# Kernel optimization log

Hardware: AMD Instinct MI355X
Metric: run time of the kernel (lower is better)

## Reference

```python
import jax, jax.numpy as jnp
import numpy as np

EPS = 1e-5
K = 20
NEG_SLOPE = 0.2


def lrelu(x):
    return jnp.where(x >= 0, x, NEG_SLOPE * x)


def bn_train(x, w, b, axes):
    # training-mode batch norm (biased variance), channel axis = 1
    m = jnp.mean(x, axis=axes, keepdims=True)
    v = jnp.mean((x - m) ** 2, axis=axes, keepdims=True)
    shp = [1] * x.ndim
    shp[1] = -1
    return (x - m) * jax.lax.rsqrt(v + EPS) * w.reshape(shp) + b.reshape(shp)


def knn_idx(x, k):
    # x: [B, C, N] -> idx [B, N, k] of k nearest neighbors (max of -dist^2)
    inner = -2.0 * jnp.einsum('bcn,bcm->bnm', x, x)
    xx = jnp.sum(x * x, axis=1)  # [B, N]
    pd = -xx[:, None, :] - inner - xx[:, :, None]  # [B, N, N]
    return jax.lax.top_k(pd, k)[1]


def graph_feature(x, k):
    # x: [B, C, N] -> [B, 2C, N, k] = cat(neighbor - center, center)
    B = x.shape[0]
    idx = knn_idx(x, k)  # [B, N, k]
    xt = jnp.transpose(x, (0, 2, 1))  # [B, N, C]
    nbr = xt[jnp.arange(B)[:, None, None], idx]  # [B, N, k, C] gather
    ctr = jnp.broadcast_to(xt[:, :, None, :], nbr.shape)
    feat = jnp.concatenate([nbr - ctr, ctr], axis=-1)  # [B, N, k, 2C]
    return jnp.transpose(feat, (0, 3, 1, 2))


def edge_conv(x, w, bw, bb):
    # EdgeConv: graph feature -> 1x1 conv (no bias) -> BN -> LeakyReLU -> max over k
    f = graph_feature(x, K)                      # [B, 2C, N, k]
    y = jnp.einsum('bcnk,oc->bonk', f, w)        # 1x1 conv2d
    y = lrelu(bn_train(y, bw, bb, (0, 2, 3)))
    return jnp.max(y, axis=-1)                   # [B, O, N]


def setup_inputs() -> dict:
    key = jax.random.key(0)
    ks = jax.random.split(key, 12)
    B, N = 8, 1024
    s = 0.05
    inp = {'x': jax.random.normal(ks[0], (B, 3, N), dtype=jnp.float32)}
    inp['c1w'] = jax.random.normal(ks[1], (64, 6), dtype=jnp.float32) * s
    inp['c2w'] = jax.random.normal(ks[2], (64, 128), dtype=jnp.float32) * s
    inp['c3w'] = jax.random.normal(ks[3], (128, 128), dtype=jnp.float32) * s
    inp['c4w'] = jax.random.normal(ks[4], (256, 256), dtype=jnp.float32) * s
    inp['c5w'] = jax.random.normal(ks[5], (1024, 512), dtype=jnp.float32) * s
    for i, c in zip(range(1, 8), [64, 64, 128, 256, 1024, 512, 256]):
        inp[f'b{i}w'] = jnp.ones((c,), dtype=jnp.float32)
        inp[f'b{i}b'] = jnp.zeros((c,), dtype=jnp.float32)
    inp['l1w'] = jax.random.normal(ks[6], (512, 2048), dtype=jnp.float32) * s
    inp['l1b'] = jnp.zeros((512,), dtype=jnp.float32)
    inp['l2w'] = jax.random.normal(ks[7], (256, 512), dtype=jnp.float32) * s
    inp['l2b'] = jnp.zeros((256,), dtype=jnp.float32)
    inp['l3w'] = jax.random.normal(ks[8], (40, 256), dtype=jnp.float32) * s
    inp['l3b'] = jnp.zeros((40,), dtype=jnp.float32)
    return inp


def reference(x, c1w, c2w, c3w, c4w, c5w,
              b1w, b1b, b2w, b2b, b3w, b3b, b4w, b4b, b5w, b5b,
              b6w, b6b, b7w, b7b,
              l1w, l1b, l2w, l2b, l3w, l3b):
    x1 = edge_conv(x, c1w, b1w, b1b)    # [B, 64, N]
    x2 = edge_conv(x1, c2w, b2w, b2b)   # [B, 64, N]
    x3 = edge_conv(x2, c3w, b3w, b3b)   # [B, 128, N]
    x4 = edge_conv(x3, c4w, b4w, b4b)   # [B, 256, N]
    cat = jnp.concatenate([x1, x2, x3, x4], axis=1)  # [B, 512, N]
    y = jnp.einsum('bcn,oc->bon', cat, c5w)          # conv5 (1x1)
    y = lrelu(bn_train(y, b5w, b5b, (0, 2)))         # [B, 1024, N]
    feat = jnp.concatenate([jnp.max(y, axis=-1), jnp.mean(y, axis=-1)], axis=1)  # [B, 2048]
    h = feat @ l1w.T + l1b
    h = lrelu(bn_train(h, b6w, b6b, (0,)))
    h = h @ l2w.T + l2b
    h = lrelu(bn_train(h, b7w, b7b, (0,)))
    return h @ l3w.T + l3b  # [B, num_class]
```

## Files before the change

### kernel.cpp

```cpp
#include <hip/hip_runtime.h>
#include <math.h>

#define NPTS 1024
#define NBATCH 8
#define KNN 20
#define KC 24
#define EPSBN 1e-5f
#define NSLOPE 0.2f

typedef __attribute__((ext_vector_type(8))) short short8_t;
typedef __attribute__((ext_vector_type(4))) float floatx4;

__device__ __forceinline__ float lrelu_f(float x){ return x >= 0.f ? x : NSLOPE*x; }

__device__ __forceinline__ unsigned short f2bf_rne(float f){
  union { float f; unsigned u; } x; x.f = f;
  unsigned r = x.u + 0x7FFFu + ((x.u >> 16) & 1u);
  return (unsigned short)(r >> 16);
}
__device__ __forceinline__ float bf2f(unsigned short h){
  union { float f; unsigned u; } x; x.u = ((unsigned)h) << 16;
  return x.f;
}

__global__ __launch_bounds__(256) void prep(const float* __restrict__ X, long bstride, int coff,
                                            int C, int Cp,
                                            unsigned short* __restrict__ Sh,
                                            unsigned short* __restrict__ Sl,
                                            float* __restrict__ XT, float* __restrict__ XX){
  __shared__ float tile[128][33];
  __shared__ float part[32][8];
  int b = blockIdx.y;
  int n0 = blockIdx.x * 32;
  int t = threadIdx.x;
  int r = t >> 3, q = t & 7;
  for (int c0 = 0; c0 < C; c0 += 32){
    int row = c0 + r;
    if (row < C){
      float4 rv = *(const float4*)(X + (size_t)b*bstride + (size_t)(coff+row)*NPTS + n0 + q*4);
      tile[row][q*4+0] = rv.x; tile[row][q*4+1] = rv.y;
      tile[row][q*4+2] = rv.z; tile[row][q*4+3] = rv.w;
    }
  }
  __syncthreads();
  size_t bn = (size_t)b*NPTS + n0 + r;
  for (int c0 = 0; c0 < Cp; c0 += 32){
    int c = c0 + q*4;
    float f0 = (c+0 < C) ? tile[c+0][r] : 0.f;
    float f1 = (c+1 < C) ? tile[c+1][r] : 0.f;
    float f2 = (c+2 < C) ? tile[c+2][r] : 0.f;
    float f3 = (c+3 < C) ? tile[c+3][r] : 0.f;
    if (C >= 32 && c < C)
      *(float4*)(XT + bn*C + c) = make_float4(f0,f1,f2,f3);
    ushort4 oh, ol;
    oh.x = f2bf_rne(f0); ol.x = f2bf_rne(f0 - bf2f(oh.x));
    oh.y = f2bf_rne(f1); ol.y = f2bf_rne(f1 - bf2f(oh.y));
    oh.z = f2bf_rne(f2); ol.z = f2bf_rne(f2 - bf2f(oh.z));
    oh.w = f2bf_rne(f3); ol.w = f2bf_rne(f3 - bf2f(oh.w));
    *(ushort4*)(Sh + bn*Cp + c) = oh;
    *(ushort4*)(Sl + bn*Cp + c) = ol;
  }
  float s = 0.f;
  for (int c = q; c < C; c += 8){ float v = tile[c][r]; s += v*v; }
  part[r][q] = s;
  __syncthreads();
  if (q == 0){
    float s8 = 0.f;
    #pragma unroll
    for (int i = 0; i < 8; ++i) s8 += part[r][i];
    XX[(size_t)b*NPTS + n0 + r] = s8;
  }
}

#define LROW 40
__global__ __launch_bounds__(256) void pd_mfma64(
    const unsigned short* __restrict__ Sh, const unsigned short* __restrict__ Sl,
    int Cp, const float* __restrict__ XX, float* __restrict__ PD){
  __shared__ __align__(16) unsigned short Ah[64*LROW];
  __shared__ __align__(16) unsigned short Al[64*LROW];
  __shared__ __align__(16) unsigned short Bh[64*LROW];
  __shared__ __align__(16) unsigned short Bl[64*LROW];
  int b  = blockIdx.z;
  int n0 = blockIdx.x * 64;
  int m0 = blockIdx.y * 64;
  int t = threadIdx.x;
  int lane = t & 63, wid = t >> 6;
  int wm = (wid & 1) * 32;
  int wn = (wid >> 1) * 32;
  int fr = lane & 15;
  int fq = (lane >> 4) * 8;
  floatx4 acc[2][2];
  #pragma unroll
  for (int i = 0; i < 2; ++i)
    #pragma unroll
    for (int j = 0; j < 2; ++j) acc[i][j] = (floatx4)(0.f);

  int srow = t >> 2, spart = (t & 3)*8;
  for (int k0 = 0; k0 < Cp; k0 += 32){
    size_t ga = ((size_t)b*NPTS + m0 + srow)*Cp + k0 + spart;
    size_t gb = ((size_t)b*NPTS + n0 + srow)*Cp + k0 + spart;
    *(short8_t*)&Ah[srow*LROW + spart] = *(const short8_t*)&Sh[ga];
    *(short8_t*)&Al[srow*LROW + spart] = *(const short8_t*)&Sl[ga];
    *(short8_t*)&Bh[srow*LROW + spart] = *(const short8_t*)&Sh[gb];
    *(short8_t*)&Bl[srow*LROW + spart] = *(const short8_t*)&Sl[gb];
    __syncthreads();
    short8_t afh[2], afl[2], bfh[2], bfl[2];
    #pragma unroll
    for (int mi = 0; mi < 2; ++mi){
      int r = (wm + mi*16 + fr)*LROW + fq;
      afh[mi] = *(const short8_t*)&Ah[r];
      afl[mi] = *(const short8_t*)&Al[r];
    }
    #pragma unroll
    for (int ni = 0; ni < 2; ++ni){
      int r = (wn + ni*16 + fr)*LROW + fq;
      bfh[ni] = *(const short8_t*)&Bh[r];
      bfl[ni] = *(const short8_t*)&Bl[r];
    }
    #pragma unroll
    for (int mi = 0; mi < 2; ++mi)
      #pragma unroll
      for (int ni = 0; ni < 2; ++ni){
        acc[mi][ni] = __builtin_amdgcn_mfma_f32_16x16x32_bf16(afh[mi], bfh[ni], acc[mi][ni], 0, 0, 0);
        acc[mi][ni] = __builtin_amdgcn_mfma_f32_16x16x32_bf16(afl[mi], bfh[ni], acc[mi][ni], 0, 0, 0);
        acc[mi][ni] = __builtin_amdgcn_mfma_f32_16x16x32_bf16(afh[mi], bfl[ni], acc[mi][ni], 0, 0, 0);
      }
    __syncthreads();
  }
  int col = lane & 15;
  int rquad = (lane >> 4) * 4;
  #pragma unroll
  for (int mi = 0; mi < 2; ++mi)
    #pragma unroll
    for (int ni = 0; ni < 2; ++ni){
      int n = n0 + wn + ni*16 + col;
      int mbase = m0 + wm + mi*16 + rquad;
      float4 xx4 = *(const float4*)(XX + (size_t)b*NPTS + mbase);
      floatx4 a = acc[mi][ni];
      float4 o = make_float4(2.f*a.x - xx4.x, 2.f*a.y - xx4.y,
                             2.f*a.z - xx4.z, 2.f*a.w - xx4.w);
      *(float4*)(PD + ((size_t)b*NPTS + n)*NPTS + mbase) = o;
    }
}

__global__ __launch_bounds__(256) void topk_refine(const float* __restrict__ PD,
                                                   const float* __restrict__ X, long bstride,
                                                   int coff, int C,
                                                   const float* __restrict__ XT,
                                                   int* __restrict__ IDX){
  int wid = threadIdx.x >> 6;
  int lane = threadIdx.x & 63;
  int row = blockIdx.x*4 + wid;
  int b = row >> 10, n = row & 1023;
  const float* p = PD + (size_t)row*NPTS;
  unsigned key[16];
  #pragma unroll
  for (int j4 = 0; j4 < 4; ++j4){
    float4 t4 = *(const float4*)&p[lane*16 + j4*4];
    float tv[4] = {t4.x, t4.y, t4.z, t4.w};
    #pragma unroll
    for (int e = 0; e < 4; ++e){
      int j = j4*4 + e;
      unsigned u = __float_as_uint(tv[e]);
      unsigned msk = (unsigned)(((int)u) >> 31) | 0x80000000u;
      key[j] = ((u ^ msk) & 0xFFFFFFF0u) | (unsigned)j;
    }
  }
  #pragma unroll
  for (int ksz = 2; ksz <= 16; ksz <<= 1){
    #pragma unroll
    for (int jj = ksz >> 1; jj > 0; jj >>= 1){
      #pragma unroll
      for (int i = 0; i < 16; ++i){
        int l = i ^ jj;
        if (l > i){
          unsigned a = key[i], c = key[l];
          unsigned mx = a > c ? a : c, mn = a > c ? c : a;
          bool maxfirst = ((i & ksz) == 0);
          key[i] = maxfirst ? mx : mn;
          key[l] = maxfirst ? mn : mx;
        }
      }
    }
  }
  int my_m = 0;
  #pragma unroll
  for (int k = 0; k < KC; ++k){
    unsigned h = key[0];
    unsigned g = h, o;
    o = (unsigned)__builtin_amdgcn_update_dpp(0, (int)g, 0x121, 0xF, 0xF, true);
    g = o > g ? o : g;
    o = (unsigned)__builtin_amdgcn_update_dpp(0, (int)g, 0x122, 0xF, 0xF, true);
    g = o > g ? o : g;
    o = (unsigned)__builtin_amdgcn_update_dpp(0, (int)g, 0x124, 0xF, 0xF, true);
    g = o > g ? o : g;
    o = (unsigned)__builtin_amdgcn_update_dpp(0, (int)g, 0x128, 0xF, 0xF, true);
    g = o > g ? o : g;
    o = (unsigned)__builtin_amdgcn_ds_swizzle((int)g, 0x401F);
    g = o > g ? o : g;
    o = (unsigned)__shfl_xor((int)g, 32, 64);
    g = o > g ? o : g;
    unsigned long long ball = __ballot(h == g);
    int wl = __ffsll(ball) - 1;
    if ((lane & 31) == k) my_m = wl*16 + (int)(g & 15u);
    bool isw = (lane == wl);
    #pragma unroll
    for (int i2 = 0; i2 < 15; ++i2) key[i2] = isw ? key[i2+1] : key[i2];
    key[15] = isw ? 0u : key[15];
  }
  int lk = lane & 31;
  double pdv = -1e300; int midx = (1 << 20) + lane;
  if (lk < KC){
    midx = my_m;
    double dot = 0.0, m2 = 0.0, n2 = 0.0;
    if (C == 3){
      if (lane < 32){
        const float* Xb = X + (size_t)b*bstride + (size_t)coff*NPTS;
        #pragma unroll
        for (int c = 0; c < 3; ++c){
          double xn = (double)Xb[(size_t)c*NPTS + n];
          double xm = (double)Xb[(size_t)c*NPTS + my_m];
          dot += xn*xm; m2 += xm*xm; n2 += xn*xn;
        }
      }
    } else {
      int C2 = C >> 1;
      int cbeg = (lane < 32) ? 0 : C2;
      int cend = (lane < 32) ? C2 : C;
      const float* rn = XT + ((size_t)b*NPTS + n)*C;
      const float* rm = XT + ((size_t)b*NPTS + my_m)*C;
      for (int c = cbeg; c < cend; c += 4){
        float4 xn4 = *(const float4*)&rn[c];
        float4 xm4 = *(const float4*)&rm[c];
        dot += (double)xn4.x*(double)xm4.x + (double)xn4.y*(double)xm4.y
             + (double)xn4.z*(double)xm4.z + (double)xn4.w*(double)xm4.w;
        m2  += (double)xm4.x*(double)xm4.x + (double)xm4.y*(double)xm4.y
             + (double)xm4.z*(double)xm4.z + (double)xm4.w*(double)xm4.w;
        n2  += (double)xn4.x*(double)xn4.x + (double)xn4.y*(double)xn4.y
             + (double)xn4.z*(double)xn4.z + (double)xn4.w*(double)xn4.w;
      }
    }
    double od = __shfl_xor(dot, 32, 64);
    double om = __shfl_xor(m2, 32, 64);
    double on = __shfl_xor(n2, 32, 64);
    dot += od; m2 += om; n2 += on;
    pdv = (2.0*dot - m2) - n2;
  }
  int rank = 0;
  #pragma unroll
  for (int j = 0; j < KC; ++j){
    double ov = __shfl(pdv, j, 64);
    int    oi = __shfl(midx, j, 64);
    rank += (ov > pdv || (ov == pdv && oi < midx)) ? 1 : 0;
  }
  if (lane < KC && rank < KNN) IDX[(size_t)row*KNN + rank] = midx;
}

__global__ __launch_bounds__(256) void lin_gemm64(const float* __restrict__ W, int M, int Cdim,
                                                  int lda, int O,
                                                  const float* __restrict__ X, long bstride,
                                                  int coff, float* __restrict__ OUT){
  __shared__ float As[16][68];
  __shared__ float Bs[16][68];
  int b = blockIdx.z;
  int m0 = blockIdx.y * 64;
  int n0 = blockIdx.x * 64;
  int t = threadIdx.x;
  const float* Xb = X + (size_t)b*bstride + (size_t)coff*NPTS;
  float acc[4][4] = {};
  int lr = t >> 4, lc = (t & 15) << 2;
  int tr = (t >> 4) << 2, tc = (t & 15) << 2;
  for (int k0 = 0; k0 < Cdim; k0 += 16){
    int c = k0 + lr;
    float4 av = make_float4(0,0,0,0);
    if (c < Cdim){
      #pragma unroll
      for (int j = 0; j < 4; ++j){
        int m = m0 + lc + j;
        float aval = (m < O) ? W[(size_t)m*lda + c]
                             : W[(size_t)(m-O)*lda + Cdim + c] - W[(size_t)(m-O)*lda + c];
        ((float*)&av)[j] = aval;
      }
    }
    float4 bv = make_float4(0,0,0,0);
    if (c < Cdim)
      bv = *(const float4*)(Xb + (size_t)c*NPTS + n0 + lc);
    *(float4*)&As[lr][lc] = av;
    *(float4*)&Bs[lr][lc] = bv;
    __syncthreads();
    #pragma unroll
    for (int kk = 0; kk < 16; ++kk){
      float4 a4 = *(const float4*)&As[kk][tr];
      float4 b4 = *(const float4*)&Bs[kk][tc];
      float a[4] = {a4.x,a4.y,a4.z,a4.w};
      float bb[4] = {b4.x,b4.y,b4.z,b4.w};
      #pragma unroll
      for (int i = 0; i < 4; ++i)
        #pragma unroll
        for (int j = 0; j < 4; ++j) acc[i][j] += a[i]*bb[j];
    }
    __syncthreads();
  }
  #pragma unroll
  for (int i = 0; i < 4; ++i){
    int m = m0 + tr + i;
    *(float4*)(OUT + ((size_t)b*M + m)*NPTS + n0 + tc) =
        make_float4(acc[i][0],acc[i][1],acc[i][2],acc[i][3]);
  }
}

__global__ void edge_stats(const float* __restrict__ V, const int* __restrict__ IDX, int O,
                           float* __restrict__ YMX, float* __restrict__ YMN,
                           float* __restrict__ S1P, float* __restrict__ S2P){
  __shared__ float vrow[NPTS];
  __shared__ float urow[NPTS];
  __shared__ float r1[256];
  __shared__ float r2[256];
  int b = blockIdx.x / O;
  int o = blockIdx.x % O;
  int t = threadIdx.x;
  const float* vp = V + ((size_t)b*2*O + o)*NPTS;
  const float* up = V + ((size_t)b*2*O + O + o)*NPTS;
  for (int i = 0; i < 4; ++i){ vrow[t+256*i] = vp[t+256*i]; urow[t+256*i] = up[t+256*i]; }
  __syncthreads();
  float s1 = 0.f, s2 = 0.f;
  size_t obase = ((size_t)b*O + o)*NPTS;
  for (int i = 0; i < 4; ++i){
    int n = t + 256*i;
    float un = urow[n];
    const int* ip = IDX + ((size_t)b*NPTS + n)*KNN;
    float mx = -1e38f, mn = 1e38f;
    #pragma unroll
    for (int k = 0; k < KNN; ++k){
      float val = un + vrow[ip[k]];
      mx = fmaxf(mx, val); mn = fminf(mn, val);
      s1 += val; s2 += val*val;
    }
    YMX[obase + n] = mx;
    YMN[obase + n] = mn;
  }
  r1[t] = s1; r2[t] = s2;
  __syncthreads();
  for (int s = 128; s > 0; s >>= 1){
    if (t < s){ r1[t] += r1[t+s]; r2[t] += r2[t+s]; }
    __syncthreads();
  }
  if (t == 0){ S1P[b*O + o] = r1[0]; S2P[b*O + o] = r2[0]; }
}

__global__ void edge_apply(const float* __restrict__ YMX, const float* __restrict__ YMN,
                           const float* __restrict__ S1P, const float* __restrict__ S2P,
                           const float* __restrict__ gw, const float* __restrict__ gb,
                           int O, float* __restrict__ CAT, int coff_out){
  int g = blockIdx.x*blockDim.x + threadIdx.x;
  int n = g & (NPTS-1);
  int o = (g >> 10) % O;
  int b = (g >> 10) / O;
  float s1 = 0.f, s2 = 0.f;
  #pragma unroll
  for (int i = 0; i < NBATCH; ++i){ s1 += S1P[i*O + o]; s2 += S2P[i*O + o]; }
  const float cnt = (float)(NBATCH*NPTS*KNN);
  float mean = s1 / cnt;
  float var = fmaxf(s2 / cnt - mean*mean, 0.f);
  float sc = gw[o] * rsqrtf(var + EPSBN);
  float sh = gb[o] - mean*sc;
  float v = (sc >= 0.f) ? YMX[g] : YMN[g];
  CAT[((size_t)b*512 + coff_out + o)*NPTS + n] = lrelu_f(sc*v + sh);
}

__global__ void wsplit(const float* __restrict__ W, int nelem,
                       unsigned short* __restrict__ Wh, unsigned short* __restrict__ Wl){
  int i = blockIdx.x*blockDim.x + threadIdx.x;
  if (i >= nelem) return;
  float f = W[i];
  unsigned short hi = f2bf_rne(f);
  Wh[i] = hi;
  Wl[i] = f2bf_rne(f - bf2f(hi));
}

__global__ void catsplit_t(const float* __restrict__ CAT,
                           unsigned short* __restrict__ Th, unsigned short* __restrict__ Tl){
  __shared__ float tile[32][33];
  int b = blockIdx.z;
  int c0 = blockIdx.y * 32;
  int n0 = blockIdx.x * 32;
  int t = threadIdx.x;
  int r = t >> 3, q = t & 7;
  float4 rv = *(const float4*)(CAT + ((size_t)b*512 + c0 + r)*NPTS + n0 + q*4);
  tile[r][q*4+0] = rv.x; tile[r][q*4+1] = rv.y; tile[r][q*4+2] = rv.z; tile[r][q*4+3] = rv.w;
  __syncthreads();
  ushort4 oh, ol;
  float f0 = tile[q*4+0][r], f1 = tile[q*4+1][r], f2 = tile[q*4+2][r], f3 = tile[q*4+3][r];
  oh.x = f2bf_rne(f0); ol.x = f2bf_rne(f0 - bf2f(oh.x));
  oh.y = f2bf_rne(f1); ol.y = f2bf_rne(f1 - bf2f(oh.y));
  oh.z = f2bf_rne(f2); ol.z = f2bf_rne(f2 - bf2f(oh.z));
  oh.w = f2bf_rne(f3); ol.w = f2bf_rne(f3 - bf2f(oh.w));
  size_t ob = ((size_t)b*NPTS + n0 + r)*512 + c0 + q*4;
  *(ushort4*)(Th + ob) = oh;
  *(ushort4*)(Tl + ob) = ol;
}

__global__ __launch_bounds__(256) void conv5_mfma(
    const unsigned short* __restrict__ Ath, const unsigned short* __restrict__ Atl,
    const unsigned short* __restrict__ Wh,  const unsigned short* __restrict__ Wl,
    float* __restrict__ OUT){
  __shared__ __align__(16) unsigned short Ah[128*LROW];
  __shared__ __align__(16) unsigned short Al[128*LROW];
  __shared__ __align__(16) unsigned short Bh[128*LROW];
  __shared__ __align__(16) unsigned short Bl[128*LROW];
  int b  = blockIdx.z;
  int n0 = blockIdx.x * 128;
  int m0 = blockIdx.y * 128;
  int t = threadIdx.x;
  int lane = t & 63, wid = t >> 6;
  int wn = (wid & 1) * 64;
  int wm = (wid >> 1) * 64;
  int fr = lane & 15;
  int fq = (lane >> 4) * 8;
  floatx4 acc[4][4];
  #pragma unroll
  for (int i = 0; i < 4; ++i)
    #pragma unroll
    for (int j = 0; j < 4; ++j) acc[i][j] = (floatx4)(0.f);

  for (int k0 = 0; k0 < 512; k0 += 32){
    #pragma unroll
    for (int c = 0; c < 2; ++c){
      int ch = t + 256*c;
      int row = ch >> 2, part = (ch & 3)*8;
      size_t ga = ((size_t)b*NPTS + n0 + row)*512 + k0 + part;
      size_t gb = ((size_t)(m0 + row))*512 + k0 + part;
      *(short8_t*)&Ah[row*LROW + part] = *(const short8_t*)&Ath[ga];
      *(short8_t*)&Al[row*LROW + part] = *(const short8_t*)&Atl[ga];
      *(short8_t*)&Bh[row*LROW + part] = *(const short8_t*)&Wh[gb];
      *(short8_t*)&Bl[row*LROW + part] = *(const short8_t*)&Wl[gb];
    }
    __syncthreads();
    short8_t afh[4], afl[4], bfh[4], bfl[4];
    #pragma unroll
    for (int ni = 0; ni < 4; ++ni){
      int r = (wn + ni*16 + fr)*LROW + fq;
      afh[ni] = *(const short8_t*)&Ah[r];
      afl[ni] = *(const short8_t*)&Al[r];
    }
    #pragma unroll
    for (int mi = 0; mi < 4; ++mi){
      int r = (wm + mi*16 + fr)*LROW + fq;
      bfh[mi] = *(const short8_t*)&Bh[r];
      bfl[mi] = *(const short8_t*)&Bl[r];
    }
    #pragma unroll
    for (int ni = 0; ni < 4; ++ni)
      #pragma unroll
      for (int mi = 0; mi < 4; ++mi){
        acc[ni][mi] = __builtin_amdgcn_mfma_f32_16x16x32_bf16(afh[ni], bfh[mi], acc[ni][mi], 0, 0, 0);
        acc[ni][mi] = __builtin_amdgcn_mfma_f32_16x16x32_bf16(afl[ni], bfh[mi], acc[ni][mi], 0, 0, 0);
        acc[ni][mi] = __builtin_amdgcn_mfma_f32_16x16x32_bf16(afh[ni], bfl[mi], acc[ni][mi], 0, 0, 0);
      }
    __syncthreads();
  }
  int col = lane & 15;
  int rquad = (lane >> 4) * 4;
  #pragma unroll
  for (int ni = 0; ni < 4; ++ni)
    #pragma unroll
    for (int mi = 0; mi < 4; ++mi){
      int m = m0 + wm + mi*16 + col;
      int n = n0 + wn + ni*16 + rquad;
      *(floatx4*)(OUT + ((size_t)b*1024 + m)*NPTS + n) = acc[ni][mi];
    }
}

__global__ void y5_stats(const float* __restrict__ Y5, float* __restrict__ S1, float* __restrict__ S2){
  __shared__ float r1[256], r2[256];
  int o = blockIdx.x;
  int t = threadIdx.x;
  float s1 = 0.f, s2 = 0.f;
  for (int b = 0; b < NBATCH; ++b){
    const float* p = Y5 + ((size_t)b*1024 + o)*NPTS;
    for (int n = t; n < NPTS; n += 256){ float v = p[n]; s1 += v; s2 += v*v; }
  }
  r1[t] = s1; r2[t] = s2;
  __syncthreads();
  for (int s = 128; s > 0; s >>= 1){
    if (t < s){ r1[t] += r1[t+s]; r2[t] += r2[t+s]; }
    __syncthreads();
  }
  if (t == 0){ S1[o] = r1[0]; S2[o] = r2[0]; }
}

__global__ void head_kernel(const float* __restrict__ Y5, const float* __restrict__ S1,
                            const float* __restrict__ S2,
                            const float* __restrict__ gw, const float* __restrict__ gb,
                            float* __restrict__ FEAT){
  __shared__ float rm[256], rs[256];
  int o = blockIdx.x & 1023;
  int b = blockIdx.x >> 10;
  int t = threadIdx.x;
  const float cnt = (float)(NBATCH*NPTS);
  float mean = S1[o] / cnt;
  float var = fmaxf(S2[o] / cnt - mean*mean, 0.f);
  float s = gw[o] * rsqrtf(var + EPSBN);
  float sh = gb[o] - mean*s;
  const float* p = Y5 + ((size_t)b*1024 + o)*NPTS;
  float mx = -1e38f, sm = 0.f;
  for (int n = t; n < NPTS; n += 256){
    float v = lrelu_f(s*p[n] + sh);
    mx = fmaxf(mx, v); sm += v;
  }
  rm[t] = mx; rs[t] = sm;
  __syncthreads();
  for (int st = 128; st > 0; st >>= 1){
    if (t < st){ rm[t] = fmaxf(rm[t], rm[t+st]); rs[t] += rs[t+st]; }
    __syncthreads();
  }
  if (t == 0){
    FEAT[(size_t)b*2048 + o]        = rm[0];
    FEAT[(size_t)b*2048 + 1024 + o] = rs[0] * (1.f/NPTS);
  }
}

__global__ void fc_bn(const float* __restrict__ IN, int ID, int OD,
                      const float* __restrict__ W, const float* __restrict__ bias,
                      const float* __restrict__ gw, const float* __restrict__ gb,
                      float* __restrict__ OUT){
  __shared__ float red[256][8];
  int f = blockIdx.x;
  int t = threadIdx.x;
  float acc[8] = {};
  const float* wr = W + (size_t)f*ID;
  for (int j = t; j < ID; j += 256){
    float wv = wr[j];
    #pragma unroll
    for (int b = 0; b < 8; ++b) acc[b] += IN[b*ID + j] * wv;
  }
  #pragma unroll
  for (int b = 0; b < 8; ++b) red[t][b] = acc[b];
  __syncthreads();
  for (int s = 128; s > 0; s >>= 1){
    if (t < s){
      #pragma unroll
      for (int b = 0; b < 8; ++b) red[t][b] += red[t+s][b];
    }
    __syncthreads();
  }
  if (t == 0){
    float h[8], mean = 0.f;
    #pragma unroll
    for (int b = 0; b < 8; ++b){ h[b] = red[0][b] + bias[f]; mean += h[b]; }
    mean *= 0.125f;
    float var = 0.f;
    #pragma unroll
    for (int b = 0; b < 8; ++b){ float d = h[b]-mean; var += d*d; }
    var *= 0.125f;
    float sc = gw[f]*rsqrtf(var + EPSBN);
    float sh = gb[f] - mean*sc;
    #pragma unroll
    for (int b = 0; b < 8; ++b) OUT[b*OD + f] = lrelu_f(sc*h[b] + sh);
  }
}

__global__ void fc_out(const float* __restrict__ IN, const float* __restrict__ W,
                       const float* __restrict__ bias, float* __restrict__ OUT){
  __shared__ float red[256][8];
  int j = blockIdx.x;
  int t = threadIdx.x;
  float wv = W[(size_t)j*256 + t];
  #pragma unroll
  for (int b = 0; b < 8; ++b) red[t][b] = IN[b*256 + t] * wv;
  __syncthreads();
  for (int s = 128; s > 0; s >>= 1){
    if (t < s){
      #pragma unroll
      for (int b = 0; b < 8; ++b) red[t][b] += red[t+s][b];
    }
    __syncthreads();
  }
  if (t == 0){
    #pragma unroll
    for (int b = 0; b < 8; ++b) OUT[b*40 + j] = red[0][b] + bias[j];
  }
}

extern "C" void kernel_launch(void* const* d_in, const int* in_sizes, int n_in,
                              void* d_out, int out_size, void* d_ws, size_t ws_size,
                              hipStream_t stream) {
  const float* x   = (const float*)d_in[0];
  const float* cw[5] = { (const float*)d_in[1], (const float*)d_in[2], (const float*)d_in[3],
                         (const float*)d_in[4], (const float*)d_in[5] };
  const float* bw[7]; const float* bbv[7];
  for (int i = 0; i < 7; ++i){ bw[i] = (const float*)d_in[6+2*i]; bbv[i] = (const float*)d_in[7+2*i]; }
  const float* l1w = (const float*)d_in[20]; const float* l1b = (const float*)d_in[21];
  const float* l2w = (const float*)d_in[22]; const float* l2b = (const float*)d_in[23];
  const float* l3w = (const float*)d_in[24]; const float* l3b = (const float*)d_in[25];
  float* out = (float*)d_out;

  float* ws = (float*)d_ws;
  float* PD    = ws;
  float* V     = ws;
  float* YMX   = ws + 4194304;
  float* YMN   = ws + 6291456;
  float* Y5    = ws;
  float* XT    = ws + 8388608;
  unsigned short* XSH = (unsigned short*)(ws + 9437184);
  unsigned short* XSL = (unsigned short*)(ws + 9961472);
  float* XX    = ws + 10485760;
  unsigned short* CATth = (unsigned short*)(ws + 8388608);
  unsigned short* CATtl = (unsigned short*)(ws + 10485760);
  unsigned short* WhP   = (unsigned short*)(ws + 12582912);
  unsigned short* WlP   = (unsigned short*)(ws + 12845056);
  float* CAT   = ws + 16777216;
  int*   IDX   = (int*)(ws + 20987904);
  float* S1P   = ws + 21151744;
  float* S2P   = ws + 21159936;
  float* FEAT  = ws + 21170176;
  float* H1    = ws + 21186560;
  float* H2    = ws + 21190656;

  struct L { int C, Cp, O; const float* in; long bs; int ci; const float* w; int bn; int co; };
  L ls[4] = {
    { 3,   32,  64, x,   (long)3*NPTS,   0,   cw[0], 0, 0   },
    { 64,  64,  64, CAT, (long)512*NPTS, 0,   cw[1], 1, 64  },
    { 64,  64, 128, CAT, (long)512*NPTS, 64,  cw[2], 2, 128 },
    { 128, 128,256, CAT, (long)512*NPTS, 128, cw[3], 3, 256 },
  };

  for (int li = 0; li < 4; ++li){
    L& l = ls[li];
    prep<<<dim3(32, NBATCH), 256, 0, stream>>>(l.in, l.bs, l.ci, l.C, l.Cp, XSH, XSL, XT, XX);
    pd_mfma64<<<dim3(16,16,NBATCH), 256, 0, stream>>>(XSH, XSL, l.Cp, XX, PD);
    topk_refine<<<(NBATCH*NPTS)/4, 256, 0, stream>>>(PD, l.in, l.bs, l.ci, l.C, XT, IDX);
    lin_gemm64<<<dim3(16, (2*l.O)/64, NBATCH), 256, 0, stream>>>(
        l.w, 2*l.O, l.C, 2*l.C, l.O, l.in, l.bs, l.ci, V);
    edge_stats<<<NBATCH*l.O, 256, 0, stream>>>(V, IDX, l.O, YMX, YMN, S1P, S2P);
    edge_apply<<<(NBATCH*l.O*NPTS)/256, 256, 0, stream>>>(
        YMX, YMN, S1P, S2P, bw[l.bn], bbv[l.bn], l.O, CAT, l.co);
  }

  wsplit<<<(1024*512+255)/256, 256, 0, stream>>>(cw[4], 1024*512, WhP, WlP);
  catsplit_t<<<dim3(32,16,NBATCH), 256, 0, stream>>>(CAT, CATth, CATtl);
  conv5_mfma<<<dim3(8,8,NBATCH), 256, 0, stream>>>(CATth, CATtl, WhP, WlP, Y5);

  y5_stats<<<1024, 256, 0, stream>>>(Y5, S1P, S2P);
  head_kernel<<<NBATCH*1024, 256, 0, stream>>>(Y5, S1P, S2P, bw[4], bbv[4], FEAT);

  fc_bn<<<512, 256, 0, stream>>>(FEAT, 2048, 512, l1w, l1b, bw[5], bbv[5], H1);
  fc_bn<<<256, 256, 0, stream>>>(H1, 512, 256, l2w, l2b, bw[6], bbv[6], H2);
  fc_out<<<40, 256, 0, stream>>>(H2, l3w, l3b, out);
}
```

Baseline: 479.8 us.

## Precompute sort keys in distance GEMM, LDS rank exchange, smaller conv5 tiles

The pairwise-distance kernel now emits packed sortable keys (float bits flipped, index in the low nibble) instead of raw floats, so the top-k kernel loads keys directly and skips the conversion. The rank computation in top-k reads candidate values from shared memory instead of doing 48 wave shuffles. Separately, conv5's output tile shrinks from 128x128 to 128x64, doubling the grid to raise occupancy and block count at the cost of reloading the A tile twice as often. The local index in the key is built from rquad within the 16-column fragment, which has to match the lane*16+j position the top-k decode expects.

```diff
diff --git a/kernel.cpp b/kernel.cpp
--- a/kernel.cpp
+++ b/kernel.cpp
@@ -21,6 +21,11 @@
 __device__ __forceinline__ float bf2f(unsigned short h){
   union { float f; unsigned u; } x; x.u = ((unsigned)h) << 16;
   return x.f;
+}
+__device__ __forceinline__ unsigned sortkey(float f, int j){
+  unsigned u = __float_as_uint(f);
+  unsigned msk = (unsigned)(((int)u) >> 31) | 0x80000000u;
+  return ((u ^ msk) & 0xFFFFFFF0u) | (unsigned)j;
 }
 
 __global__ __launch_bounds__(256) void prep(const float* __restrict__ X, long bstride, int coff,
@@ -75,7 +80,7 @@
 #define LROW 40
 __global__ __launch_bounds__(256) void pd_mfma64(
     const unsigned short* __restrict__ Sh, const unsigned short* __restrict__ Sl,
-    int Cp, const float* __restrict__ XX, float* __restrict__ PD){
+    int Cp, const float* __restrict__ XX, unsigned* __restrict__ PD){
   __shared__ __align__(16) unsigned short Ah[64*LROW];
   __shared__ __align__(16) unsigned short Al[64*LROW];
   __shared__ __align__(16) unsigned short Bh[64*LROW];
@@ -137,34 +142,32 @@
       int mbase = m0 + wm + mi*16 + rquad;
       float4 xx4 = *(const float4*)(XX + (size_t)b*NPTS + mbase);
       floatx4 a = acc[mi][ni];
-      float4 o = make_float4(2.f*a.x - xx4.x, 2.f*a.y - xx4.y,
-                             2.f*a.z - xx4.z, 2.f*a.w - xx4.w);
-      *(float4*)(PD + ((size_t)b*NPTS + n)*NPTS + mbase) = o;
-    }
-}
-
-__global__ __launch_bounds__(256) void topk_refine(const float* __restrict__ PD,
+      uint4 o;
+      o.x = sortkey(2.f*a.x - xx4.x, rquad+0);
+      o.y = sortkey(2.f*a.y - xx4.y, rquad+1);
+      o.z = sortkey(2.f*a.z - xx4.z, rquad+2);
+      o.w = sortkey(2.f*a.w - xx4.w, rquad+3);
+      *(uint4*)(PD + ((size_t)b*NPTS + n)*NPTS + mbase) = o;
+    }
+}
+
+__global__ __launch_bounds__(256) void topk_refine(const unsigned* __restrict__ PD,
                                                    const float* __restrict__ X, long bstride,
                                                    int coff, int C,
                                                    const float* __restrict__ XT,
                                                    int* __restrict__ IDX){
+  __shared__ double sp[4][32];
+  __shared__ int    si[4][32];
   int wid = threadIdx.x >> 6;
   int lane = threadIdx.x & 63;
   int row = blockIdx.x*4 + wid;
   int b = row >> 10, n = row & 1023;
-  const float* p = PD + (size_t)row*NPTS;
+  const unsigned* p = PD + (size_t)row*NPTS;
   unsigned key[16];
   #pragma unroll
   for (int j4 = 0; j4 < 4; ++j4){
-    float4 t4 = *(const float4*)&p[lane*16 + j4*4];
-    float tv[4] = {t4.x, t4.y, t4.z, t4.w};
-    #pragma unroll
-    for (int e = 0; e < 4; ++e){
-      int j = j4*4 + e;
-      unsigned u = __float_as_uint(tv[e]);
-      unsigned msk = (unsigned)(((int)u) >> 31) | 0x80000000u;
-      key[j] = ((u ^ msk) & 0xFFFFFFF0u) | (unsigned)j;
-    }
+    uint4 t4 = *(const uint4*)&p[lane*16 + j4*4];
+    key[j4*4+0] = t4.x; key[j4*4+1] = t4.y; key[j4*4+2] = t4.z; key[j4*4+3] = t4.w;
   }
   #pragma unroll
   for (int ksz = 2; ksz <= 16; ksz <<= 1){
@@ -246,11 +249,12 @@
     dot += od; m2 += om; n2 += on;
     pdv = (2.0*dot - m2) - n2;
   }
+  if (lane < KC){ sp[wid][lane] = pdv; si[wid][lane] = midx; }
   int rank = 0;
   #pragma unroll
   for (int j = 0; j < KC; ++j){
-    double ov = __shfl(pdv, j, 64);
-    int    oi = __shfl(midx, j, 64);
+    double ov = sp[wid][j];
+    int    oi = si[wid][j];
     rank += (ov > pdv || (ov == pdv && oi < midx)) ? 1 : 0;
   }
   if (lane < KC && rank < KNN) IDX[(size_t)row*KNN + rank] = midx;
@@ -406,37 +410,40 @@
     float* __restrict__ OUT){
   __shared__ __align__(16) unsigned short Ah[128*LROW];
   __shared__ __align__(16) unsigned short Al[128*LROW];
-  __shared__ __align__(16) unsigned short Bh[128*LROW];
-  __shared__ __align__(16) unsigned short Bl[128*LROW];
+  __shared__ __align__(16) unsigned short Bh[64*LROW];
+  __shared__ __align__(16) unsigned short Bl[64*LROW];
   int b  = blockIdx.z;
   int n0 = blockIdx.x * 128;
-  int m0 = blockIdx.y * 128;
+  int m0 = blockIdx.y * 64;
   int t = threadIdx.x;
   int lane = t & 63, wid = t >> 6;
   int wn = (wid & 1) * 64;
-  int wm = (wid >> 1) * 64;
+  int wm = (wid >> 1) * 32;
   int fr = lane & 15;
   int fq = (lane >> 4) * 8;
-  floatx4 acc[4][4];
+  floatx4 acc[4][2];
   #pragma unroll
   for (int i = 0; i < 4; ++i)
     #pragma unroll
-    for (int j = 0; j < 4; ++j) acc[i][j] = (floatx4)(0.f);
-
+    for (int j = 0; j < 2; ++j) acc[i][j] = (floatx4)(0.f);
+
+  int srowB = t >> 2, spartB = (t & 3)*8;
   for (int k0 = 0; k0 < 512; k0 += 32){
     #pragma unroll
     for (int c = 0; c < 2; ++c){
       int ch = t + 256*c;
       int row = ch >> 2, part = (ch & 3)*8;
       size_t ga = ((size_t)b*NPTS + n0 + row)*512 + k0 + part;
-      size_t gb = ((size_t)(m0 + row))*512 + k0 + part;
       *(short8_t*)&Ah[row*LROW + part] = *(const short8_t*)&Ath[ga];
       *(short8_t*)&Al[row*LROW + part] = *(const short8_t*)&Atl[ga];
-      *(short8_t*)&Bh[row*LROW + part] = *(const short8_t*)&Wh[gb];
-      *(short8_t*)&Bl[row*LROW + part] = *(const short8_t*)&Wl[gb];
-    }
-    __syncthreads();
-    short8_t afh[4], afl[4], bfh[4], bfl[4];
+    }
+    {
+      size_t gb = ((size_t)(m0 + srowB))*512 + k0 + spartB;
+      *(short8_t*)&Bh[srowB*LROW + spartB] = *(const short8_t*)&Wh[gb];
+      *(short8_t*)&Bl[srowB*LROW + spartB] = *(const short8_t*)&Wl[gb];
+    }
+    __syncthreads();
+    short8_t afh[4], afl[4], bfh[2], bfl[2];
     #pragma unroll
     for (int ni = 0; ni < 4; ++ni){
       int r = (wn + ni*16 + fr)*LROW + fq;
@@ -444,7 +451,7 @@
       afl[ni] = *(const short8_t*)&Al[r];
     }
     #pragma unroll
-    for (int mi = 0; mi < 4; ++mi){
+    for (int mi = 0; mi < 2; ++mi){
       int r = (wm + mi*16 + fr)*LROW + fq;
       bfh[mi] = *(const short8_t*)&Bh[r];
       bfl[mi] = *(const short8_t*)&Bl[r];
@@ -452,7 +459,7 @@
     #pragma unroll
     for (int ni = 0; ni < 4; ++ni)
       #pragma unroll
-      for (int mi = 0; mi < 4; ++mi){
+      for (int mi = 0; mi < 2; ++mi){
         acc[ni][mi] = __builtin_amdgcn_mfma_f32_16x16x32_bf16(afh[ni], bfh[mi], acc[ni][mi], 0, 0, 0);
         acc[ni][mi] = __builtin_amdgcn_mfma_f32_16x16x32_bf16(afl[ni], bfh[mi], acc[ni][mi], 0, 0, 0);
         acc[ni][mi] = __builtin_amdgcn_mfma_f32_16x16x32_bf16(afh[ni], bfl[mi], acc[ni][mi], 0, 0, 0);
@@ -464,7 +471,7 @@
   #pragma unroll
   for (int ni = 0; ni < 4; ++ni)
     #pragma unroll
-    for (int mi = 0; mi < 4; ++mi){
+    for (int mi = 0; mi < 2; ++mi){
       int m = m0 + wm + mi*16 + col;
       int n = n0 + wn + ni*16 + rquad;
       *(floatx4*)(OUT + ((size_t)b*1024 + m)*NPTS + n) = acc[ni][mi];
@@ -596,7 +603,7 @@
   float* out = (float*)d_out;
 
   float* ws = (float*)d_ws;
-  float* PD    = ws;
+  unsigned* PD = (unsigned*)ws;
   float* V     = ws;
   float* YMX   = ws + 4194304;
   float* YMN   = ws + 6291456;
@@ -639,7 +646,7 @@
 
   wsplit<<<(1024*512+255)/256, 256, 0, stream>>>(cw[4], 1024*512, WhP, WlP);
   catsplit_t<<<dim3(32,16,NBATCH), 256, 0, stream>>>(CAT, CATth, CATtl);
-  conv5_mfma<<<dim3(8,8,NBATCH), 256, 0, stream>>>(CATth, CATtl, WhP, WlP, Y5);
+  conv5_mfma<<<dim3(8,16,NBATCH), 256, 0, stream>>>(CATth, CATtl, WhP, WlP, Y5);
 
   y5_stats<<<1024, 256, 0, stream>>>(Y5, S1P, S2P);
   head_kernel<<<NBATCH*1024, 256, 0, stream>>>(Y5, S1P, S2P, bw[4], bbv[4], FEAT);
```

Measured after the change: 480.8 us. About the same (+0.2%).
